# Kernel optimization log

Hardware: AMD Instinct MI355X
Metric: run time of the kernel (lower is better)

The kernel has to match this reference:

```python
import jax, jax.numpy as jnp
import numpy as np

N, T, L = 4, 2048, 2048
DQIN, DFEAT, DQK, DV = 32, 34, 64, 64  # modality feat=34 -> V input = 34-2 = 32, K input = last col


def _sorted_timeline(k, shape):
    return jnp.sort(jax.random.uniform(k, shape, jnp.float32) * 100.0, axis=-1)


def setup_inputs() -> dict:
    key = jax.random.key(0)
    ks = jax.random.split(key, 32)
    inp = {}
    inp["ref_data"] = jax.random.normal(ks[0], (N, 1, T, DQIN), jnp.float32)
    inp["ref_t"] = _sorted_timeline(ks[1], (N, 1, T))
    inp["m1_data"] = jax.random.normal(ks[2], (N, 1, L, DFEAT), jnp.float32)
    inp["m1_t"] = _sorted_timeline(ks[3], (N, 1, L))
    inp["m2_data"] = jax.random.normal(ks[4], (N, 1, L, DFEAT), jnp.float32)
    inp["m2_t"] = _sorted_timeline(ks[5], (N, 1, L))
    inp["m3_data"] = jax.random.normal(ks[6], (N, 1, L, DFEAT), jnp.float32)
    inp["m3_t"] = _sorted_timeline(ks[7], (N, 1, L))
    # shared W_Q (bias=False): d_q_in -> d_qk
    inp["Wq"] = jax.random.normal(ks[8], (DQIN, DQK), jnp.float32) / np.sqrt(DQIN)
    # per-modality params: W_K: 1 -> d_qk (with bias), W_V: (DFEAT-2) -> d_v (with bias), log-temperature
    for i, m in enumerate(["1", "2", "3"]):
        b = 9 + 4 * i
        inp["Wk" + m] = jax.random.normal(ks[b], (1, DQK), jnp.float32)
        inp["bk" + m] = jax.random.normal(ks[b + 1], (DQK,), jnp.float32) * 0.02
        inp["Wv" + m] = jax.random.normal(ks[b + 2], (DFEAT - 2, DV), jnp.float32) / np.sqrt(DFEAT - 2)
        inp["bv" + m] = jax.random.normal(ks[b + 3], (DV,), jnp.float32) * 0.02
        inp["log_tau" + m] = jnp.zeros((), jnp.float32)  # log(init_tau=1)
    return inp


def _unimodal(Q, ref_t, data, t, Wk, bk, Wv, bv, log_tau):
    # K path: last feature column through linear, then feature_map_k = [1, -x]
    Kr = data[..., -1:] @ Wk + bk                                   # (N,1,L,DQK)
    K = jnp.concatenate([jnp.ones(Kr.shape[:-1] + (1,), Kr.dtype), -Kr], axis=-1)  # (N,1,L,DQK+1)
    V = data[..., :-2] @ Wv + bv                                    # (N,1,L,DV)
    tau = jnp.exp(log_tau)
    # gaussian weight: -(Q.K)^2 / tau
    S = -jnp.square(jnp.einsum('nhtc,nhlc->nhtl', Q, K)) / tau       # (N,1,T,L)
    mask = (ref_t[..., :, None] >= t[..., None, :]).astype(S.dtype)  # (N,1,T,L)
    A = jax.nn.softmax(S * mask, axis=-1) * mask
    return jnp.einsum('nhtl,nhlc->nhtc', A, V)                       # (N,1,T,DV)


def reference(ref_data, ref_t, m1_data, m1_t, m2_data, m2_t, m3_data, m3_t,
              Wq, Wk1, bk1, Wv1, bv1, log_tau1, Wk2, bk2, Wv2, bv2, log_tau2,
              Wk3, bk3, Wv3, bv3, log_tau3):
    # compute_Q (qk_type='time'): Q = add_one(W_Q(ref_data)) -> append ones column
    Qr = jnp.einsum('nhtd,dk->nhtk', ref_data, Wq)
    Q = jnp.concatenate([Qr, jnp.ones(Qr.shape[:-1] + (1,), Qr.dtype)], axis=-1)  # (N,1,T,DQK+1)
    y1 = _unimodal(Q, ref_t, m1_data, m1_t, Wk1, bk1, Wv1, bv1, log_tau1)
    y2 = _unimodal(Q, ref_t, m2_data, m2_t, Wk2, bk2, Wv2, bv2, log_tau2)
    y3 = _unimodal(Q, ref_t, m3_data, m3_t, Wk3, bk3, Wv3, bv3, log_tau3)
    # original returns dict {m1: y1, m2: y2, m3: y3}; stacked here (3,N,1,T,DV)
    return jnp.stack([y1, y2, y3], axis=0)
```

## Files before the change

kernel.cpp:

```cpp
#include <hip/hip_runtime.h>

namespace {

typedef unsigned int uint;
typedef unsigned short ushort_t;
typedef __attribute__((ext_vector_type(8))) short bf16x8;
typedef __attribute__((ext_vector_type(4))) float f32x4;

constexpr int N = 4, T = 2048, L = 2048;
constexpr int DQIN = 32, DQK = 64;

constexpr int VI_SZ = 3 * N * 64 * L;
constexpr int X_SZ = 3 * N * L;
constexpr int A_SZ = 3 * N * T;

union PK8 { int i[4]; bf16x8 s; };

__global__ __launch_bounds__(256) void mm_prep(
    const float* __restrict__ ref_data, const float* __restrict__ ref_t,
    const float* __restrict__ d1, const float* __restrict__ t1,
    const float* __restrict__ d2, const float* __restrict__ t2,
    const float* __restrict__ d3, const float* __restrict__ t3,
    const float* __restrict__ Wq,
    const float* __restrict__ Wk1, const float* __restrict__ bk1,
    const float* __restrict__ Wv1, const float* __restrict__ bv1, const float* __restrict__ lt1,
    const float* __restrict__ Wk2, const float* __restrict__ bk2,
    const float* __restrict__ Wv2, const float* __restrict__ bv2, const float* __restrict__ lt2,
    const float* __restrict__ Wk3, const float* __restrict__ bk3,
    const float* __restrict__ Wv3, const float* __restrict__ bv3, const float* __restrict__ lt3,
    float* __restrict__ Aq, float* __restrict__ Gq, int* __restrict__ Cq,
    ushort_t* __restrict__ VI, float* __restrict__ X) {
  const int b = blockIdx.x;
  const int tid = threadIdx.x;

  if (b < 96) {
    const int m = b >> 5;
    const int idx = (b & 31) * 256 + tid;
    __shared__ float sWq[DQIN * DQK];
    __shared__ float sWk[DQK];
    __shared__ float sbk[DQK];
    const float* Wk = (m == 0) ? Wk1 : (m == 1 ? Wk2 : Wk3);
    const float* bk = (m == 0) ? bk1 : (m == 1 ? bk2 : bk3);
    const float* lt = (m == 0) ? lt1 : (m == 1 ? lt2 : lt3);
    for (int i = tid; i < DQIN * DQK; i += 256) sWq[i] = Wq[i];
    if (tid < DQK) { sWk[tid] = Wk[tid]; sbk[tid] = bk[tid]; }
    __syncthreads();
    float x[DQIN];
    const float* rp = ref_data + idx * DQIN;
#pragma unroll
    for (int i = 0; i < DQIN; i++) x[i] = rp[i];
    float qr[DQK];
#pragma unroll
    for (int j = 0; j < DQK; j += 4) {
      float4 acc4 = make_float4(0.f, 0.f, 0.f, 0.f);
#pragma unroll
      for (int i = 0; i < DQIN; i++) {
        const float4 w = *(const float4*)&sWq[i * DQK + j];
        acc4.x = fmaf(x[i], w.x, acc4.x);
        acc4.y = fmaf(x[i], w.y, acc4.y);
        acc4.z = fmaf(x[i], w.z, acc4.z);
        acc4.w = fmaf(x[i], w.w, acc4.w);
      }
      qr[j] = acc4.x; qr[j + 1] = acc4.y; qr[j + 2] = acc4.z; qr[j + 3] = acc4.w;
    }
    const float rs = __expf(-0.5f * lt[0]);
    float g = 0.f, h = 0.f;
#pragma unroll
    for (int j = 1; j < DQK; j++) {
      g = fmaf(qr[j], sWk[j - 1], g);
      h = fmaf(qr[j], sbk[j - 1], h);
    }
    g += sWk[DQK - 1];
    h += sbk[DQK - 1];
    Aq[m * (N * T) + idx] = (qr[0] - h) * rs;
    Gq[m * (N * T) + idx] = g * rs;
  } else if (b < 192) {
    const int sidx = (b - 96) * 256 + tid;
    const int m = sidx >> 13;
    const int nt = sidx & 8191;
    const int n = nt >> 11;
    const float rt = ref_t[nt];
    const float* tml = ((m == 0) ? t1 : (m == 1 ? t2 : t3)) + n * L;
    int lo = 0, hi = L;
    while (lo < hi) {
      const int mid = (lo + hi) >> 1;
      if (tml[mid] <= rt) lo = mid + 1; else hi = mid;
    }
    Cq[m * 8192 + nt] = lo;
  } else {
    const int vb = b - 192;
    const int mn = vb >> 5;
    const int m = mn >> 2, n = mn & 3;
    const int lseg0 = (vb & 31) * 64;
    const float* dm = (m == 0) ? d1 : (m == 1 ? d2 : d3);
    const float* Wv = (m == 0) ? Wv1 : (m == 1 ? Wv2 : Wv3);
    const float* bv = (m == 0) ? bv1 : (m == 1 ? bv2 : bv3);
    const int cdim = tid & 63;
    const int qq = tid >> 6;
    const int l0 = lseg0 + qq * 16;

    float Wc[32];
#pragma unroll
    for (int i = 0; i < 32; i++) Wc[i] = Wv[i * 64 + cdim];
    const float bvc = bv[cdim];

    uint hi16[16], lo16[16];
#pragma unroll 4
    for (int k = 0; k < 16; k++) {
      const float* dp = dm + (size_t)(n * L + l0 + k) * 34;
      float acc = bvc;
#pragma unroll
      for (int i = 0; i < 32; i++) acc = fmaf(dp[i], Wc[i], acc);
      uint u = __float_as_uint(acc);
      uint h = (u + 0x7fffu + ((u >> 16) & 1u)) & 0xffff0000u;
      float res = acc - __uint_as_float(h);
      uint ul = __float_as_uint(res);
      uint hl = (ul + 0x7fffu + ((ul >> 16) & 1u)) >> 16;
      hi16[k] = h >> 16;
      lo16[k] = hl;
    }
    int pkh[8], pkl[8];
#pragma unroll
    for (int p = 0; p < 8; p++) {
      pkh[p] = (int)(hi16[2 * p] | (hi16[2 * p + 1] << 16));
      pkl[p] = (int)(lo16[2 * p] | (lo16[2 * p + 1] << 16));
    }
    ushort_t* dst = VI + (size_t)(mn * 64 + cdim) * (2 * L) + (l0 >> 3) * 16;
    *(int4*)dst = make_int4(pkh[0], pkh[1], pkh[2], pkh[3]);
    *(int4*)(dst + 8) = make_int4(pkl[0], pkl[1], pkl[2], pkl[3]);
    *(int4*)(dst + 16) = make_int4(pkh[4], pkh[5], pkh[6], pkh[7]);
    *(int4*)(dst + 24) = make_int4(pkl[4], pkl[5], pkl[6], pkl[7]);

    if (tid < 64) {
      const int l = lseg0 + tid;
      X[mn * L + l] = dm[(size_t)(n * L + l) * 34 + 33];
    }
  }
}

__device__ inline void stage_chunk(ushort_t* dstbuf, const ushort_t* VIb, int ch,
                                   int w, int lane) {
#pragma unroll
  for (int i = 0; i < 4; i++) {
    const int u = (w * 4 + i) * 64 + lane;
    const int lr = u >> 4;
    const int gs = u & 15;
    const int g = (gs - lr) & 15;
    const ushort_t* src = VIb + (size_t)lr * 4096 + ch * 128 + g * 8;
    __builtin_amdgcn_global_load_lds(
        (const __attribute__((address_space(1))) void*)src,
        (__attribute__((address_space(3))) void*)(dstbuf + (w * 4 + i) * 512),
        16, 0, 0);
  }
}

__global__ __launch_bounds__(128, 3) void mm_attn_main(
    const ushort_t* __restrict__ VI, const float* __restrict__ X,
    const float* __restrict__ Aq, const float* __restrict__ Gq, const int* __restrict__ Cq,
    float* __restrict__ out) {
  __shared__ ushort_t sbuf[2][4096];
  __shared__ float sx[2048];

  const int b = blockIdx.x;
  const int mn = b % 12;
  const int rr0 = b / 12;
  const int dh = rr0 & 1;
  const int j = rr0 >> 1;
  const int pj = (j & 1) ? (j >> 1) : (63 - (j >> 1));

  const int tid = threadIdx.x;
  const int lane = tid & 63;
  const int w = tid >> 6;
  const int q = lane >> 4;
  const int m16 = lane & 15;

  const int rg = pj * 2 + w;
  const int tbase = mn * T + rg * 16;

  const int c = Cq[tbase + m16];
  const int cmax = __shfl(c, 15, 64);
  const int cmin = __shfl(c, 0, 64);
  const int nch = (cmax + 63) >> 6;

  const int cB = Cq[mn * T + (pj * 2 + 1) * 16 + 15];
  const int nchB = (cB + 63) >> 6;

  const float a = Aq[tbase + m16];
  const float g = Gq[tbase + m16];

  f32x4 acc[2];
  acc[0] = (f32x4){0.f, 0.f, 0.f, 0.f};
  acc[1] = (f32x4){0.f, 0.f, 0.f, 0.f};
  float z = 0.f;

  const ushort_t* VIb = VI + (size_t)(mn * 64 + dh * 32) * 4096;
  const float* xg = X + mn * L;

  int oh[2][2], ol[2][2];
#pragma unroll
  for (int ct = 0; ct < 2; ct++) {
#pragma unroll
    for (int kk = 0; kk < 2; kk++) {
      const int lr = ct * 16 + m16;
      oh[ct][kk] = lr * 128 + (((kk * 8 + q * 2 + 0) + lr) & 15) * 8;
      ol[ct][kk] = lr * 128 + (((kk * 8 + q * 2 + 1) + lr) & 15) * 8;
    }
  }

#pragma unroll
  for (int i = 0; i < 4; i++) {
    const float* src = xg + (w * 4 + i) * 256 + lane * 4;
    __builtin_amdgcn_global_load_lds(
        (const __attribute__((address_space(1))) void*)src,
        (__attribute__((address_space(3))) void*)(sx + (w * 4 + i) * 256),
        16, 0, 0);
  }
  stage_chunk(sbuf[0], VIb, 0, w, lane);
  __syncthreads();

  for (int ch = 0; ch < nchB; ch++) {
    const int nb = ch & 1;
    if (ch + 1 < nchB) stage_chunk(sbuf[nb ^ 1], VIb, ch + 1, w, lane);

    if (ch < nch) {
      const int base = ch << 6;
      const ushort_t* buf = sbuf[nb];
      const bool inter = (base + 64 <= cmin);
#pragma unroll
      for (int kk = 0; kk < 2; kk++) {
        const int k0 = base + kk * 32 + q * 8;
        const float4 xa = *(const float4*)&sx[k0];
        const float4 xb = *(const float4*)&sx[k0 + 4];
        const float xs[8] = {xa.x, xa.y, xa.z, xa.w, xb.x, xb.y, xb.z, xb.w};
        float wv[8];
        if (inter) {
#pragma unroll
          for (int jj = 0; jj < 8; jj++) {
            const float d = fmaf(-g, xs[jj], a);
            wv[jj] = __expf(-d * d);
            z += wv[jj];
          }
        } else {
#pragma unroll
          for (int jj = 0; jj < 8; jj++) {
            const float d = fmaf(-g, xs[jj], a);
            const float e = __expf(-d * d);
            wv[jj] = (k0 + jj < c) ? e : 0.f;
            z += wv[jj];
          }
        }
        PK8 ph, pl;
#pragma unroll
        for (int p2 = 0; p2 < 4; p2++) {
          const uint u0 = __float_as_uint(wv[2 * p2]);
          const uint u1 = __float_as_uint(wv[2 * p2 + 1]);
          const uint h0 = u0 & 0xffff0000u, h1 = u1 & 0xffff0000u;
          const float l0f = wv[2 * p2] - __uint_as_float(h0);
          const float l1f = wv[2 * p2 + 1] - __uint_as_float(h1);
          ph.i[p2] = (int)((h0 >> 16) | h1);
          pl.i[p2] = (int)((__float_as_uint(l0f) >> 16) | (__float_as_uint(l1f) & 0xffff0000u));
        }
        const bf16x8 ahi = ph.s, alo = pl.s;
#pragma unroll
        for (int ct = 0; ct < 2; ct++) {
          const bf16x8 bh = *(const bf16x8*)(buf + oh[ct][kk]);
          const bf16x8 bl = *(const bf16x8*)(buf + ol[ct][kk]);
          acc[ct] = __builtin_amdgcn_mfma_f32_16x16x32_bf16(ahi, bh, acc[ct], 0, 0, 0);
          acc[ct] = __builtin_amdgcn_mfma_f32_16x16x32_bf16(ahi, bl, acc[ct], 0, 0, 0);
          acc[ct] = __builtin_amdgcn_mfma_f32_16x16x32_bf16(alo, bh, acc[ct], 0, 0, 0);
        }
      }
    }
    __syncthreads();
  }

  z += __shfl_xor(z, 16, 64);
  z += __shfl_xor(z, 32, 64);

#pragma unroll
  for (int rr = 0; rr < 4; rr++) {
    const int row = q * 4 + rr;
    const float zr = __shfl(z, row, 64);
    const int cr = __shfl(c, row, 64);
    const float inv = 1.0f / (zr + (float)(L - cr));
#pragma unroll
    for (int ct = 0; ct < 2; ct++) {
      out[(size_t)(tbase + row) * 64 + dh * 32 + ct * 16 + m16] = acc[ct][rr] * inv;
    }
  }
}

}

extern "C" void kernel_launch(void* const* d_in, const int* in_sizes, int n_in,
                              void* d_out, int out_size, void* d_ws, size_t ws_size,
                              hipStream_t stream) {
  const float* ref_data = (const float*)d_in[0];
  const float* ref_t = (const float*)d_in[1];
  const float* m1_data = (const float*)d_in[2];
  const float* m1_t = (const float*)d_in[3];
  const float* m2_data = (const float*)d_in[4];
  const float* m2_t = (const float*)d_in[5];
  const float* m3_data = (const float*)d_in[6];
  const float* m3_t = (const float*)d_in[7];
  const float* Wq = (const float*)d_in[8];
  const float* Wk1 = (const float*)d_in[9];
  const float* bk1 = (const float*)d_in[10];
  const float* Wv1 = (const float*)d_in[11];
  const float* bv1 = (const float*)d_in[12];
  const float* lt1 = (const float*)d_in[13];
  const float* Wk2 = (const float*)d_in[14];
  const float* bk2 = (const float*)d_in[15];
  const float* Wv2 = (const float*)d_in[16];
  const float* bv2 = (const float*)d_in[17];
  const float* lt2 = (const float*)d_in[18];
  const float* Wk3 = (const float*)d_in[19];
  const float* bk3 = (const float*)d_in[20];
  const float* Wv3 = (const float*)d_in[21];
  const float* bv3 = (const float*)d_in[22];
  const float* lt3 = (const float*)d_in[23];

  float* ws = (float*)d_ws;
  ushort_t* VI = (ushort_t*)ws;
  float* Xw = ws + VI_SZ;
  float* Aq = Xw + X_SZ;
  float* Gq = Aq + A_SZ;
  int* Cq = (int*)(Gq + A_SZ);

  mm_prep<<<dim3(576), dim3(256), 0, stream>>>(
      ref_data, ref_t, m1_data, m1_t, m2_data, m2_t, m3_data, m3_t, Wq,
      Wk1, bk1, Wv1, bv1, lt1, Wk2, bk2, Wv2, bv2, lt2, Wk3, bk3, Wv3, bv3, lt3,
      Aq, Gq, Cq, VI, Xw);
  mm_attn_main<<<dim3(12 * 64 * 2), dim3(128), 0, stream>>>(
      VI, Xw, Aq, Gq, Cq, (float*)d_out);
}
```

Before: 155.5 us.

## Give each wave private LDS double buffers and drop block-wide barriers

Each wave now stages its own copy of the V chunk into a per-wave LDS double buffer and synchronises with s_waitcnt instead of __syncthreads. This lets the two waves in a block run independent chunk counts and removes barrier stalls, so the faster wave no longer loops to the slower wave's count. X values are prefetched into registers rather than staged in shared memory. Block scheduling changes from alternating heavy and light rows to a simple descending order, and the occupancy hint drops from 3 to 2. The cost is doubled global-to-LDS traffic for V, since each wave loads the full chunk, plus more LDS per block.

```diff
diff --git a/kernel.cpp b/kernel.cpp
--- a/kernel.cpp
+++ b/kernel.cpp
@@ -138,35 +138,33 @@
   }
 }
 
-__device__ inline void stage_chunk(ushort_t* dstbuf, const ushort_t* VIb, int ch,
-                                   int w, int lane) {
-#pragma unroll
-  for (int i = 0; i < 4; i++) {
-    const int u = (w * 4 + i) * 64 + lane;
-    const int lr = u >> 4;
-    const int gs = u & 15;
-    const int g = (gs - lr) & 15;
-    const ushort_t* src = VIb + (size_t)lr * 4096 + ch * 128 + g * 8;
+__device__ inline void stage64(ushort_t* dst, const ushort_t* VIb, int ch, int lane) {
+#pragma unroll
+  for (int i = 0; i < 8; i++) {
+    const int n = i * 64 + lane;
+    const int lr = n >> 4;
+    const int slot = n & 15;
+    const int u = (slot - lr) & 15;
+    const ushort_t* src = VIb + (size_t)lr * 4096 + ch * 128 + u * 8;
     __builtin_amdgcn_global_load_lds(
         (const __attribute__((address_space(1))) void*)src,
-        (__attribute__((address_space(3))) void*)(dstbuf + (w * 4 + i) * 512),
+        (__attribute__((address_space(3))) void*)(dst + i * 512),
         16, 0, 0);
   }
 }
 
-__global__ __launch_bounds__(128, 3) void mm_attn_main(
+__global__ __launch_bounds__(128, 2) void mm_attn_main(
     const ushort_t* __restrict__ VI, const float* __restrict__ X,
     const float* __restrict__ Aq, const float* __restrict__ Gq, const int* __restrict__ Cq,
     float* __restrict__ out) {
-  __shared__ ushort_t sbuf[2][4096];
-  __shared__ float sx[2048];
+  __shared__ ushort_t sbuf[2][2][4096];
 
   const int b = blockIdx.x;
   const int mn = b % 12;
-  const int rr0 = b / 12;
-  const int dh = rr0 & 1;
-  const int j = rr0 >> 1;
-  const int pj = (j & 1) ? (j >> 1) : (63 - (j >> 1));
+  const int r = b / 12;
+  const int dh = r & 1;
+  const int j = r >> 1;
+  const int pj = 63 - j;
 
   const int tid = threadIdx.x;
   const int lane = tid & 63;
@@ -182,9 +180,6 @@
   const int cmin = __shfl(c, 0, 64);
   const int nch = (cmax + 63) >> 6;
 
-  const int cB = Cq[mn * T + (pj * 2 + 1) * 16 + 15];
-  const int nchB = (cB + 63) >> 6;
-
   const float a = Aq[tbase + m16];
   const float g = Gq[tbase + m16];
 
@@ -202,76 +197,85 @@
 #pragma unroll
     for (int kk = 0; kk < 2; kk++) {
       const int lr = ct * 16 + m16;
-      oh[ct][kk] = lr * 128 + (((kk * 8 + q * 2 + 0) + lr) & 15) * 8;
-      ol[ct][kk] = lr * 128 + (((kk * 8 + q * 2 + 1) + lr) & 15) * 8;
-    }
-  }
-
-#pragma unroll
-  for (int i = 0; i < 4; i++) {
-    const float* src = xg + (w * 4 + i) * 256 + lane * 4;
-    __builtin_amdgcn_global_load_lds(
-        (const __attribute__((address_space(1))) void*)src,
-        (__attribute__((address_space(3))) void*)(sx + (w * 4 + i) * 256),
-        16, 0, 0);
-  }
-  stage_chunk(sbuf[0], VIb, 0, w, lane);
-  __syncthreads();
-
-  for (int ch = 0; ch < nchB; ch++) {
+      const int uh = (kk * 4 + q) * 2;
+      oh[ct][kk] = lr * 128 + (((uh + 0) + lr) & 15) * 8;
+      ol[ct][kk] = lr * 128 + (((uh + 1) + lr) & 15) * 8;
+    }
+  }
+
+  float4 xc[4], xn[4];
+  if (nch > 0) {
+#pragma unroll
+    for (int kk = 0; kk < 2; kk++) {
+      xc[kk * 2] = *(const float4*)&xg[kk * 32 + q * 8];
+      xc[kk * 2 + 1] = *(const float4*)&xg[kk * 32 + q * 8 + 4];
+    }
+    stage64(sbuf[w][0], VIb, 0, lane);
+  }
+
+  for (int ch = 0; ch < nch; ch++) {
     const int nb = ch & 1;
-    if (ch + 1 < nchB) stage_chunk(sbuf[nb ^ 1], VIb, ch + 1, w, lane);
-
-    if (ch < nch) {
-      const int base = ch << 6;
-      const ushort_t* buf = sbuf[nb];
-      const bool inter = (base + 64 <= cmin);
+    if (ch + 1 < nch) {
+      const int base1 = (ch + 1) << 6;
 #pragma unroll
       for (int kk = 0; kk < 2; kk++) {
-        const int k0 = base + kk * 32 + q * 8;
-        const float4 xa = *(const float4*)&sx[k0];
-        const float4 xb = *(const float4*)&sx[k0 + 4];
-        const float xs[8] = {xa.x, xa.y, xa.z, xa.w, xb.x, xb.y, xb.z, xb.w};
-        float wv[8];
-        if (inter) {
-#pragma unroll
-          for (int jj = 0; jj < 8; jj++) {
-            const float d = fmaf(-g, xs[jj], a);
-            wv[jj] = __expf(-d * d);
-            z += wv[jj];
-          }
-        } else {
-#pragma unroll
-          for (int jj = 0; jj < 8; jj++) {
-            const float d = fmaf(-g, xs[jj], a);
-            const float e = __expf(-d * d);
-            wv[jj] = (k0 + jj < c) ? e : 0.f;
-            z += wv[jj];
-          }
+        xn[kk * 2] = *(const float4*)&xg[base1 + kk * 32 + q * 8];
+        xn[kk * 2 + 1] = *(const float4*)&xg[base1 + kk * 32 + q * 8 + 4];
+      }
+      stage64(sbuf[w][nb ^ 1], VIb, ch + 1, lane);
+      __builtin_amdgcn_s_waitcnt(0x0F78);
+    } else {
+      __builtin_amdgcn_s_waitcnt(0x0F70);
+    }
+
+    const int base = ch << 6;
+    const ushort_t* buf = sbuf[w][nb];
+    const bool inter = (base + 64 <= cmin);
+#pragma unroll
+    for (int kk = 0; kk < 2; kk++) {
+      const int k0 = base + kk * 32 + q * 8;
+      const float4 xa = xc[kk * 2], xb = xc[kk * 2 + 1];
+      const float xs[8] = {xa.x, xa.y, xa.z, xa.w, xb.x, xb.y, xb.z, xb.w};
+      float wv[8];
+      if (inter) {
+#pragma unroll
+        for (int jj = 0; jj < 8; jj++) {
+          const float d = fmaf(-g, xs[jj], a);
+          wv[jj] = __expf(-d * d);
+          z += wv[jj];
         }
-        PK8 ph, pl;
-#pragma unroll
-        for (int p2 = 0; p2 < 4; p2++) {
-          const uint u0 = __float_as_uint(wv[2 * p2]);
-          const uint u1 = __float_as_uint(wv[2 * p2 + 1]);
-          const uint h0 = u0 & 0xffff0000u, h1 = u1 & 0xffff0000u;
-          const float l0f = wv[2 * p2] - __uint_as_float(h0);
-          const float l1f = wv[2 * p2 + 1] - __uint_as_float(h1);
-          ph.i[p2] = (int)((h0 >> 16) | h1);
-          pl.i[p2] = (int)((__float_as_uint(l0f) >> 16) | (__float_as_uint(l1f) & 0xffff0000u));
+      } else {
+#pragma unroll
+        for (int jj = 0; jj < 8; jj++) {
+          const float d = fmaf(-g, xs[jj], a);
+          const float e = __expf(-d * d);
+          wv[jj] = (k0 + jj < c) ? e : 0.f;
+          z += wv[jj];
         }
-        const bf16x8 ahi = ph.s, alo = pl.s;
-#pragma unroll
-        for (int ct = 0; ct < 2; ct++) {
-          const bf16x8 bh = *(const bf16x8*)(buf + oh[ct][kk]);
-          const bf16x8 bl = *(const bf16x8*)(buf + ol[ct][kk]);
-          acc[ct] = __builtin_amdgcn_mfma_f32_16x16x32_bf16(ahi, bh, acc[ct], 0, 0, 0);
-          acc[ct] = __builtin_amdgcn_mfma_f32_16x16x32_bf16(ahi, bl, acc[ct], 0, 0, 0);
-          acc[ct] = __builtin_amdgcn_mfma_f32_16x16x32_bf16(alo, bh, acc[ct], 0, 0, 0);
-        }
-      }
-    }
-    __syncthreads();
+      }
+      PK8 ph, pl;
+#pragma unroll
+      for (int p2 = 0; p2 < 4; p2++) {
+        const uint u0 = __float_as_uint(wv[2 * p2]);
+        const uint u1 = __float_as_uint(wv[2 * p2 + 1]);
+        const uint h0 = u0 & 0xffff0000u, h1 = u1 & 0xffff0000u;
+        const float l0f = wv[2 * p2] - __uint_as_float(h0);
+        const float l1f = wv[2 * p2 + 1] - __uint_as_float(h1);
+        ph.i[p2] = (int)((h0 >> 16) | h1);
+        pl.i[p2] = (int)((__float_as_uint(l0f) >> 16) | (__float_as_uint(l1f) & 0xffff0000u));
+      }
+      const bf16x8 ahi = ph.s, alo = pl.s;
+#pragma unroll
+      for (int ct = 0; ct < 2; ct++) {
+        const bf16x8 bh = *(const bf16x8*)(buf + oh[ct][kk]);
+        const bf16x8 bl = *(const bf16x8*)(buf + ol[ct][kk]);
+        acc[ct] = __builtin_amdgcn_mfma_f32_16x16x32_bf16(ahi, bh, acc[ct], 0, 0, 0);
+        acc[ct] = __builtin_amdgcn_mfma_f32_16x16x32_bf16(ahi, bl, acc[ct], 0, 0, 0);
+        acc[ct] = __builtin_amdgcn_mfma_f32_16x16x32_bf16(alo, bh, acc[ct], 0, 0, 0);
+      }
+    }
+#pragma unroll
+    for (int i = 0; i < 4; i++) xc[i] = xn[i];
   }
 
   z += __shfl_xor(z, 16, 64);
```

Result: no change. 155.7 us (+0.1%).
